# Optimization experiments

Measured on AMD Instinct MI355X. Metric: run time of the kernel, lower is better.

Reference implementation:

```python
import jax, jax.numpy as jnp
import numpy as np

N_NODES = 50000
N_EDGES = 800000
N_FEAT = 128
NHID = 64
B = 512          # num graphs
K = 30           # sort-pool k
N_CLASSES = 10


def _sage(x, src, dst, Wl, bl, Wr, n):
    # PyG SAGEConv: out = lin_l(mean_{j in N(i)} x_j) + lin_r(x_i)
    deg = jax.ops.segment_sum(jnp.ones(src.shape[0], x.dtype), dst, num_segments=n)
    agg = jax.ops.segment_sum(x[src], dst, num_segments=n)
    agg = agg / jnp.maximum(deg, 1.0)[:, None]
    return agg @ Wl + bl + x @ Wr


def _sort_pool(x, batch, num_graphs, k):
    # sort nodes within each graph descending by last feature channel, keep top-k (zero pad)
    n, f = x.shape
    order = jnp.lexsort((-x[:, -1], batch))  # primary: batch asc, secondary: last-feat desc
    xs = x[order]
    bs = batch[order]
    counts = jax.ops.segment_sum(jnp.ones(n, jnp.int32), batch, num_segments=num_graphs)
    starts = jnp.concatenate([jnp.zeros(1, jnp.int32), jnp.cumsum(counts)[:-1]])
    rank = jnp.arange(n, dtype=jnp.int32) - starts[bs]
    valid = rank < k
    gidx = jnp.where(valid, bs, num_graphs)  # out-of-bounds -> dropped by scatter
    ridx = jnp.where(valid, rank, 0)
    out = jnp.zeros((num_graphs, k, f), x.dtype).at[gidx, ridx].set(xs)
    return out  # [B, k, f]


def setup_inputs() -> dict:
    key = jax.random.key(0)
    ks = jax.random.split(key, 16)
    d = {}
    d["x"] = jax.random.normal(ks[0], (N_NODES, N_FEAT), dtype=jnp.float32)
    d["edge_index"] = jax.random.randint(ks[1], (2, N_EDGES), 0, N_NODES, dtype=jnp.int64)
    d["batch"] = jnp.sort(jax.random.randint(ks[2], (N_NODES,), 0, B, dtype=jnp.int64))

    def lin(k, fan_in, shape):
        s = 1.0 / np.sqrt(fan_in)
        return jax.random.uniform(k, shape, jnp.float32, -s, s)

    d["W1l"] = lin(ks[3], N_FEAT, (N_FEAT, NHID)); d["b1"] = lin(ks[4], N_FEAT, (NHID,))
    d["W1r"] = lin(ks[5], N_FEAT, (N_FEAT, NHID))
    d["W2l"] = lin(ks[6], NHID, (NHID, NHID)); d["b2"] = lin(ks[7], NHID, (NHID,))
    d["W2r"] = lin(ks[8], NHID, (NHID, NHID))
    d["W3l"] = lin(ks[9], NHID, (NHID, NHID)); d["b3"] = lin(ks[10], NHID, (NHID,))
    d["W3r"] = lin(ks[11], NHID, (NHID, NHID))
    d["convw"] = lin(ks[12], NHID * 5, (32, NHID, 5))  # OIH
    d["convb"] = lin(ks[13], NHID * 5, (32,))
    d["lin1w"] = lin(ks[14], 32 * 26, (32 * 26, NHID)); d["lin1b"] = lin(ks[14], 32 * 26, (NHID,))
    d["lin2w"] = lin(ks[15], NHID, (NHID, N_CLASSES)); d["lin2b"] = lin(ks[15], NHID, (N_CLASSES,))
    return d


def reference(x, edge_index, batch, W1l, b1, W1r, W2l, b2, W2r, W3l, b3, W3r,
              convw, convb, lin1w, lin1b, lin2w, lin2b):
    src, dst = edge_index[0], edge_index[1]
    h = jax.nn.relu(_sage(x, src, dst, W1l, b1, W1r, N_NODES))
    h = jax.nn.relu(_sage(h, src, dst, W2l, b2, W2r, N_NODES))
    h = jax.nn.relu(_sage(h, src, dst, W3l, b3, W3r, N_NODES))
    p = _sort_pool(h, batch, B, K)            # [B, K, NHID]
    p = jnp.transpose(p, (0, 2, 1))           # [B, NHID, K]
    c = jax.lax.conv_general_dilated(p, convw, (1,), 'VALID',
                                     dimension_numbers=('NCH', 'OIH', 'NCH'))
    c = jax.nn.relu(c + convb[None, :, None])  # [B, 32, 26]
    f = c.reshape(B, -1)
    f = jax.nn.relu(f @ lin1w + lin1b)
    logits = f @ lin2w + lin2b
    return jax.nn.log_softmax(logits, axis=-1)
```

## Files before the change

kernel.cpp:

```cpp
#include <hip/hip_runtime.h>
#include <hip/hip_bf16.h>
#include <math.h>

#define NND 50000
#define NE 800000
#define NF 128
#define NH 64
#define NB 512
#define KP 30
#define NCLS 10
#define NBKT 49
#define NTILE 196
#define NG1 782
#define NSET 208

typedef __hip_bfloat16 bf16;
typedef unsigned long long u64;
typedef unsigned short ushort_t;
typedef __attribute__((ext_vector_type(8))) short bf16x8;
typedef __attribute__((ext_vector_type(4))) float f32x4;

__device__ __forceinline__ float ldF(const void* p, size_t i, int isbf){
    return isbf ? __bfloat162float(((const bf16*)p)[i]) : ((const float*)p)[i];
}

__device__ __forceinline__ ushort_t f2bf(float v){
    unsigned u = __float_as_uint(v);
    unsigned r = u + 0x7FFFu + ((u >> 16) & 1u);
    return (ushort_t)(r >> 16);
}

__device__ __forceinline__ int floatsAreBf16(const unsigned* __restrict__ xw, int tid){
    unsigned w = xw[tid & 63];
    int ex = (int)((w >> 7) & 0xFF);
    u64 m = __ballot(ex >= 100 && ex <= 140);
    return __popcll(m) >= 32;
}
__device__ __forceinline__ int intsAreI64(const int* __restrict__ ew, int tid){
    u64 m = __ballot(ew[2*(tid & 63) + 1] == 0);
    return __popcll(m) >= 48;
}

__device__ __forceinline__ int edgeSrc(const int* ei, int e, int i64){
    return i64 ? ei[2*e] : ei[e];
}
__device__ __forceinline__ int edgeDst(const int* ei, int e, int i64){
    return i64 ? ei[2*NE + 2*e] : ei[NE + e];
}

__global__ __launch_bounds__(256) void k1_kernel(
    const unsigned* __restrict__ xw, const int* __restrict__ ei,
    const int* __restrict__ batch, int* __restrict__ starts,
    const void* W1l, const void* W1r, const void* b1,
    const void* W2l, const void* W2r, const void* b2,
    const void* W3l, const void* W3r, const void* b3,
    const void* convw, const void* convb,
    const void* l1w, const void* l1b, const void* l2w, const void* l2b,
    ushort_t* __restrict__ wB1, ushort_t* __restrict__ wB2, ushort_t* __restrict__ wB3,
    float* __restrict__ b1f, float* __restrict__ b2f, float* __restrict__ b3f,
    float* __restrict__ wT, float* __restrict__ cbf,
    float* __restrict__ l1wf, float* __restrict__ l1bf,
    float* __restrict__ l2wf, float* __restrict__ l2bf,
    int* __restrict__ bcnt, int* __restrict__ dctr,
    int* __restrict__ bbase, int* __restrict__ bcur, int* __restrict__ offs)
{
    int tid = threadIdx.x;
    if (blockIdx.x < NTILE){
        __shared__ int lh[NBKT];
        __shared__ int sc[NBKT];
        __shared__ int lastFlag;
        int i64 = intsAreI64(ei, tid);
        if (tid < NBKT) lh[tid] = 0;
        __syncthreads();
        int t0 = blockIdx.x*4096;
        #pragma unroll 4
        for (int k = 0; k < 16; ++k){
            int e = t0 + k*256 + tid;
            if (e < NE) atomicAdd(&lh[edgeDst(ei,e,i64) >> 10], 1);
        }
        __syncthreads();
        if (tid < NBKT && lh[tid]) atomicAdd(&bcnt[tid], lh[tid]);
        __syncthreads();
        if (tid == 0){
            __threadfence();
            int old = atomicAdd(dctr, 1);
            lastFlag = (old == NTILE-1) ? 1 : 0;
        }
        __syncthreads();
        if (lastFlag){
            if (tid < NBKT) sc[tid] = atomicAdd(&bcnt[tid], 0);
            __syncthreads();
            if (tid == 0){
                int acc = 0;
                for (int b = 0; b < NBKT; ++b){
                    bbase[b] = acc; bcur[b] = acc; acc += sc[b];
                }
                bbase[NBKT] = acc;
                offs[NND] = NE;
            }
        }
    } else {
        int wbf = floatsAreBf16(xw, tid);
        int i64 = intsAreI64(ei, tid);
        int i = (blockIdx.x - NTILE)*256 + tid;
        if (i < NND){
            int b  = i64 ? batch[2*i] : batch[i];
            int pb = (i == 0) ? -1 : (i64 ? batch[2*(i-1)] : batch[i-1]);
            for (int g = pb+1; g <= b; ++g) starts[g] = i;
            if (i == NND-1) for (int g = b+1; g <= NB; ++g) starts[g] = NND;
        }
        {
            int j = i & 7, lane = (i >> 3) & 63, t = (i >> 9) & 7, c = i >> 12;
            int k = c*32 + (lane >> 4)*8 + j;
            int n = t*16 + (lane & 15);
            if (i < 16384){
                float v = (n < 64) ? ldF(W1l, (size_t)k*NH + n, wbf)
                                   : ldF(W1r, (size_t)k*NH + (n-64), wbf);
                wB1[i] = f2bf(v);
            }
            if (i < 8192){
                float v2 = (n < 64) ? ldF(W2l, (size_t)k*NH + n, wbf)
                                    : ldF(W2r, (size_t)k*NH + (n-64), wbf);
                float v3 = (n < 64) ? ldF(W3l, (size_t)k*NH + n, wbf)
                                    : ldF(W3r, (size_t)k*NH + (n-64), wbf);
                wB2[i] = f2bf(v2);
                wB3[i] = f2bf(v3);
            }
        }
        if (i < 64){
            b1f[i] = ldF(b1, i, wbf);
            b2f[i] = ldF(b2, i, wbf);
            b3f[i] = ldF(b3, i, wbf);
            l1bf[i] = ldF(l1b, i, wbf);
        }
        if (i < 10240){
            int o = i / 320, rem = i - o*320, ch = rem/5, h = rem - ch*5;
            wT[ch*160 + h*32 + o] = ldF(convw, i, wbf);
        }
        if (i < 53248) l1wf[i] = ldF(l1w, i, wbf);
        if (i < 640)   l2wf[i] = ldF(l2w, i, wbf);
        if (i < 32)    cbf[i]  = ldF(convb, i, wbf);
        if (i < 10)    l2bf[i] = ldF(l2b, i, wbf);
    }
}

__global__ __launch_bounds__(256) void k2_kernel(
    const void* __restrict__ x, const int* __restrict__ ei,
    const ushort_t* __restrict__ wB1, const float* __restrict__ b1f,
    ushort_t* __restrict__ ybf, float* __restrict__ z,
    int* __restrict__ bcur, int2* __restrict__ bedges)
{
    int tid = threadIdx.x;
    if (blockIdx.x < NG1){
        constexpr int K = NF, KC = K/32, RS = K + 8;
        __shared__ ushort_t hA[64*RS];
        int isbf = floatsAreBf16((const unsigned*)x, tid);
        int base = blockIdx.x * 64;
        for (int i = tid; i < 64*K; i += 256){
            int r = i / K, c = i - r*K;
            int node = base + r;
            float v = (node < NND) ? ldF(x, (size_t)node*K + c, isbf) : 0.f;
            hA[r*RS + c] = f2bf(v);
        }
        __syncthreads();
        int lane = tid & 63, w = tid >> 6;
        int n16 = lane & 15, quad = lane >> 4;
        f32x4 acc[8];
        #pragma unroll
        for (int t = 0; t < 8; ++t) acc[t] = (f32x4){0.f,0.f,0.f,0.f};
        const bf16x8* bp = (const bf16x8*)wB1;
        #pragma unroll
        for (int c = 0; c < KC; ++c){
            bf16x8 a = *(const bf16x8*)&hA[(w*16 + n16)*RS + c*32 + quad*8];
            #pragma unroll
            for (int t = 0; t < 8; ++t){
                bf16x8 b = bp[(c*8 + t)*64 + lane];
                acc[t] = __builtin_amdgcn_mfma_f32_16x16x32_bf16(a, b, acc[t], 0, 0, 0);
            }
        }
        #pragma unroll
        for (int t = 0; t < 8; ++t){
            int f = (t & 3)*16 + n16;
            float bv = (t >= 4) ? b1f[f] : 0.f;
            #pragma unroll
            for (int r = 0; r < 4; ++r){
                int node = base + w*16 + quad*4 + r;
                if (node < NND){
                    if (t < 4) ybf[(size_t)node*NH + f] = f2bf(acc[t][r]);
                    else       z[(size_t)node*NH + f] = acc[t][r] + bv;
                }
            }
        }
    } else {
        __shared__ int lh[NBKT];
        __shared__ int lcur[NBKT];
        int i64 = intsAreI64(ei, tid);
        if (tid < NBKT) lh[tid] = 0;
        __syncthreads();
        int t0 = (blockIdx.x - NG1)*4096;
        int myd[16], mys[16];
        int cnt = 0;
        #pragma unroll 4
        for (int k = 0; k < 16; ++k){
            int e = t0 + k*256 + tid;
            if (e < NE){
                int d = edgeDst(ei,e,i64), s_ = edgeSrc(ei,e,i64);
                myd[cnt] = d; mys[cnt] = s_; ++cnt;
                atomicAdd(&lh[d >> 10], 1);
            }
        }
        __syncthreads();
        if (tid < NBKT) lcur[tid] = lh[tid] ? atomicAdd(&bcur[tid], lh[tid]) : 0;
        __syncthreads();
        for (int k = 0; k < cnt; ++k){
            int b = myd[k] >> 10;
            int p = atomicAdd(&lcur[b], 1);
            bedges[p] = make_int2(mys[k], myd[k]);
        }
    }
}

__global__ __launch_bounds__(1024) void csr_finalize(const int2* __restrict__ bedges,
                                                     const int* __restrict__ bbase,
                                                     int* __restrict__ offs,
                                                     int* __restrict__ csr){
    __shared__ int hist[1024];
    int b = blockIdx.x;
    int tid = threadIdx.x;
    int dst0 = b << 10;
    int nd = NND - dst0; if (nd > 1024) nd = 1024;
    int e0 = bbase[b], e1 = bbase[b+1];
    hist[tid] = 0;
    __syncthreads();
    for (int e = e0 + tid; e < e1; e += 1024)
        atomicAdd(&hist[bedges[e].y - dst0], 1);
    __syncthreads();
    int own = hist[tid];
    for (int st = 1; st < 1024; st <<= 1){
        int v = (tid >= st) ? hist[tid-st] : 0;
        __syncthreads();
        hist[tid] += v;
        __syncthreads();
    }
    int excl = hist[tid] - own;
    if (tid < nd) offs[dst0 + tid] = e0 + excl;
    __syncthreads();
    hist[tid] = excl;
    __syncthreads();
    for (int e = e0 + tid; e < e1; e += 1024){
        int2 ed = bedges[e];
        int p = atomicAdd(&hist[ed.y - dst0], 1);
        csr[e0 + p] = ed.x;
    }
}

__device__ __forceinline__ void addbf8(uint4 u, float* a){
    a[0] += __uint_as_float(u.x << 16);
    a[1] += __uint_as_float(u.x & 0xFFFF0000u);
    a[2] += __uint_as_float(u.y << 16);
    a[3] += __uint_as_float(u.y & 0xFFFF0000u);
    a[4] += __uint_as_float(u.z << 16);
    a[5] += __uint_as_float(u.z & 0xFFFF0000u);
    a[6] += __uint_as_float(u.w << 16);
    a[7] += __uint_as_float(u.w & 0xFFFF0000u);
}

__global__ __launch_bounds__(256) void gather_mfma(
    const ushort_t* __restrict__ yb, const int* __restrict__ offs,
    const int* __restrict__ csr, const float* __restrict__ z,
    const ushort_t* __restrict__ wB, const float* __restrict__ bfp,
    ushort_t* __restrict__ ybf_out, float* __restrict__ z_out,
    ushort_t* __restrict__ ykey_out)
{
    constexpr int K = NH;
    constexpr int KC = K/32;
    constexpr int RS = K + 8;
    __shared__ ushort_t hA[64*RS];
    int tid = threadIdx.x;
    int base = blockIdx.x * 64;

    {
        int nl = tid >> 2, q = tid & 3;
        int node = base + nl;
        float acc[16];
        #pragma unroll
        for (int i = 0; i < 16; ++i) acc[i] = 0.f;
        ushort_t row[16];
        if (node < NND){
            int o0 = offs[node], o1 = offs[node+1];
            int e = o0;
            for (; e + 3 < o1; e += 4){
                int s0 = csr[e], s1 = csr[e+1], s2 = csr[e+2], s3 = csr[e+3];
                const uint4* p0 = (const uint4*)&yb[(size_t)s0*NH + q*16];
                const uint4* p1 = (const uint4*)&yb[(size_t)s1*NH + q*16];
                const uint4* p2 = (const uint4*)&yb[(size_t)s2*NH + q*16];
                const uint4* p3 = (const uint4*)&yb[(size_t)s3*NH + q*16];
                uint4 a0 = p0[0], a1 = p0[1], b0 = p1[0], b1 = p1[1];
                uint4 c0 = p2[0], c1 = p2[1], d0 = p3[0], d1 = p3[1];
                addbf8(a0, acc); addbf8(a1, acc+8);
                addbf8(b0, acc); addbf8(b1, acc+8);
                addbf8(c0, acc); addbf8(c1, acc+8);
                addbf8(d0, acc); addbf8(d1, acc+8);
            }
            for (; e < o1; ++e){
                const uint4* p0 = (const uint4*)&yb[(size_t)csr[e]*NH + q*16];
                uint4 a0 = p0[0], a1 = p0[1];
                addbf8(a0, acc); addbf8(a1, acc+8);
            }
            float dd = (float)(o1 - o0); dd = dd > 1.f ? dd : 1.f;
            float inv = 1.f / dd;
            const float4* zp = (const float4*)&z[(size_t)node*NH + q*16];
            #pragma unroll
            for (int i4 = 0; i4 < 4; ++i4){
                float4 zz = zp[i4];
                float v0 = acc[i4*4+0]*inv + zz.x;
                float v1 = acc[i4*4+1]*inv + zz.y;
                float v2 = acc[i4*4+2]*inv + zz.z;
                float v3 = acc[i4*4+3]*inv + zz.w;
                row[i4*4+0] = f2bf(v0 > 0.f ? v0 : 0.f);
                row[i4*4+1] = f2bf(v1 > 0.f ? v1 : 0.f);
                row[i4*4+2] = f2bf(v2 > 0.f ? v2 : 0.f);
                row[i4*4+3] = f2bf(v3 > 0.f ? v3 : 0.f);
            }
        } else {
            #pragma unroll
            for (int i = 0; i < 16; ++i) row[i] = 0;
        }
        unsigned pk[8];
        #pragma unroll
        for (int i = 0; i < 8; ++i)
            pk[i] = (unsigned)row[2*i] | ((unsigned)row[2*i+1] << 16);
        *(uint4*)&hA[nl*RS + q*16]     = make_uint4(pk[0],pk[1],pk[2],pk[3]);
        *(uint4*)&hA[nl*RS + q*16 + 8] = make_uint4(pk[4],pk[5],pk[6],pk[7]);
    }
    __syncthreads();

    int lane = tid & 63, w = tid >> 6;
    int n16 = lane & 15, quad = lane >> 4;
    f32x4 acc[8];
    #pragma unroll
    for (int t = 0; t < 8; ++t) acc[t] = (f32x4){0.f,0.f,0.f,0.f};
    const bf16x8* bp = (const bf16x8*)wB;
    #pragma unroll
    for (int c = 0; c < KC; ++c){
        bf16x8 a = *(const bf16x8*)&hA[(w*16 + n16)*RS + c*32 + quad*8];
        #pragma unroll
        for (int t = 0; t < 8; ++t){
            bf16x8 b = bp[(c*8 + t)*64 + lane];
            acc[t] = __builtin_amdgcn_mfma_f32_16x16x32_bf16(a, b, acc[t], 0, 0, 0);
        }
    }
    #pragma unroll
    for (int t = 0; t < 8; ++t){
        int f = (t & 3)*16 + n16;
        float bv = (t >= 4) ? bfp[f] : 0.f;
        #pragma unroll
        for (int r = 0; r < 4; ++r){
            int node = base + w*16 + quad*4 + r;
            if (node < NND){
                if (t < 4){
                    ushort_t yv = f2bf(acc[t][r]);
                    ybf_out[(size_t)node*NH + f] = yv;
                    if (ykey_out != nullptr && t == 3 && n16 == 15)
                        ykey_out[node] = yv;
                } else {
                    z_out[(size_t)node*NH + f] = acc[t][r] + bv;
                }
            }
        }
    }
}

__device__ __forceinline__ void acc4(uint2 u, float& a0, float& a1, float& a2, float& a3){
    a0 += __uint_as_float(u.x << 16);
    a1 += __uint_as_float(u.x & 0xFFFF0000u);
    a2 += __uint_as_float(u.y << 16);
    a3 += __uint_as_float(u.y & 0xFFFF0000u);
}

__global__ __launch_bounds__(256) void head4_kernel(
    const ushort_t* __restrict__ yb, const ushort_t* __restrict__ ykey,
    const int* __restrict__ offs, const int* __restrict__ csr,
    const float* __restrict__ z, const int* __restrict__ starts,
    const float* __restrict__ wT, const float* __restrict__ cbf,
    const float* __restrict__ l1wf, const float* __restrict__ l1bf,
    const float* __restrict__ l2wf, const float* __restrict__ l2bf,
    float* __restrict__ outp)
{
    __shared__ u64  keys[256];
    __shared__ int  sel[KP];
    __shared__ float pT[64*32];
    __shared__ float part[8*832];
    __shared__ float cbuf[832];
    __shared__ float fbuf[NH];
    __shared__ float logitsS[NCLS];
    int g = blockIdx.x, tid = threadIdx.x;
    int s = starts[g], e = starts[g+1];
    int cnt = e - s; if (cnt > 256) cnt = 256; if (cnt < 0) cnt = 0;

    u64 key = 0xFFFFFFFFFFFFFFFFull;
    if (tid < cnt){
        int node = s + tid;
        int o0 = offs[node], o1 = offs[node+1];
        float a = 0.f;
        int ee = o0;
        for (; ee + 3 < o1; ee += 4){
            float v0 = __uint_as_float((unsigned)ykey[csr[ee+0]] << 16);
            float v1 = __uint_as_float((unsigned)ykey[csr[ee+1]] << 16);
            float v2 = __uint_as_float((unsigned)ykey[csr[ee+2]] << 16);
            float v3 = __uint_as_float((unsigned)ykey[csr[ee+3]] << 16);
            a += v0; a += v1; a += v2; a += v3;
        }
        for (; ee < o1; ++ee)
            a += __uint_as_float((unsigned)ykey[csr[ee]] << 16);
        float dd = (float)(o1 - o0); dd = dd > 1.f ? dd : 1.f;
        float inv = 1.f / dd;
        float v = a*inv + z[(size_t)node*NH + 63];
        v = v > 0.f ? v : 0.f;
        unsigned u = __float_as_uint(v);
        unsigned m = (u & 0x80000000u) ? ~u : (u | 0x80000000u);
        unsigned d = ~m;
        key = ((u64)d << 32) | (unsigned)tid;
    }
    keys[tid] = key;
    __syncthreads();
    for (int k = 2; k <= 256; k <<= 1){
        for (int j = k >> 1; j > 0; j >>= 1){
            int partner = tid ^ j;
            u64 a = keys[tid], b = keys[partner];
            bool up = ((tid & k) == 0);
            bool amin = a < b;
            u64 keep;
            if (partner > tid) keep = (up == amin) ? a : b;
            else               keep = (up == amin) ? b : a;
            __syncthreads();
            keys[tid] = keep;
            __syncthreads();
        }
    }
    if (tid < KP){
        u64 kk = keys[tid];
        sel[tid] = ((unsigned)(kk >> 32) == 0xFFFFFFFFu) ? -1 : (int)(kk & 0xFFFFFFFFu);
    }
    if (tid < 64){ pT[tid*32 + 30] = 0.f; pT[tid*32 + 31] = 0.f; }
    __syncthreads();

    #pragma unroll
    for (int r0 = 0; r0 < 32; r0 += 16){
        int r = r0 + (tid >> 4);
        int q = tid & 15;
        if (r < KP){
            float4 v = make_float4(0.f,0.f,0.f,0.f);
            int li = sel[r];
            if (li >= 0){
                int node = s + li;
                int o0 = offs[node], o1 = offs[node+1];
                float a0=0.f, a1=0.f, a2=0.f, a3=0.f;
                int ee = o0;
                for (; ee + 3 < o1; ee += 4){
                    int s0 = csr[ee], s1 = csr[ee+1], s2 = csr[ee+2], s3 = csr[ee+3];
                    uint2 u0 = *(const uint2*)&yb[(size_t)s0*NH + q*4];
                    uint2 u1 = *(const uint2*)&yb[(size_t)s1*NH + q*4];
                    uint2 u2 = *(const uint2*)&yb[(size_t)s2*NH + q*4];
                    uint2 u3 = *(const uint2*)&yb[(size_t)s3*NH + q*4];
                    acc4(u0, a0,a1,a2,a3); acc4(u1, a0,a1,a2,a3);
                    acc4(u2, a0,a1,a2,a3); acc4(u3, a0,a1,a2,a3);
                }
                for (; ee < o1; ++ee){
                    uint2 u = *(const uint2*)&yb[(size_t)csr[ee]*NH + q*4];
                    acc4(u, a0,a1,a2,a3);
                }
                float dd = (float)(o1 - o0); dd = dd > 1.f ? dd : 1.f;
                float inv = 1.f / dd;
                float4 zz = *(const float4*)&z[(size_t)node*NH + q*4];
                v.x = a0*inv + zz.x; v.y = a1*inv + zz.y;
                v.z = a2*inv + zz.z; v.w = a3*inv + zz.w;
                v.x = v.x > 0.f ? v.x : 0.f;  v.y = v.y > 0.f ? v.y : 0.f;
                v.z = v.z > 0.f ? v.z : 0.f;  v.w = v.w > 0.f ? v.w : 0.f;
            }
            pT[(q*4+0)*32 + r] = v.x;
            pT[(q*4+1)*32 + r] = v.y;
            pT[(q*4+2)*32 + r] = v.z;
            pT[(q*4+3)*32 + r] = v.w;
        }
    }
    __syncthreads();

    int o = tid & 31, chg = tid >> 5;
    float acc[26];
    #pragma unroll
    for (int t = 0; t < 26; ++t) acc[t] = 0.f;
    for (int c8 = 0; c8 < 8; ++c8){
        int ch = chg*8 + c8;
        const float4* prow = (const float4*)&pT[ch*32];
        float p[32];
        #pragma unroll
        for (int q = 0; q < 8; ++q){
            float4 v = prow[q];
            p[4*q]=v.x; p[4*q+1]=v.y; p[4*q+2]=v.z; p[4*q+3]=v.w;
        }
        const float* wrow = &wT[ch*160 + o];
        #pragma unroll
        for (int h = 0; h < 5; ++h){
            float wv = wrow[h*32];
            #pragma unroll
            for (int t = 0; t < 26; ++t) acc[t] += p[t+h]*wv;
        }
    }
    #pragma unroll
    for (int t = 0; t < 26; ++t) part[chg*832 + o*26 + t] = acc[t];
    __syncthreads();

    for (int i = tid; i < 832; i += 256){
        int oo = i / 26;
        float a = cbf[oo];
        #pragma unroll
        for (int cg = 0; cg < 8; ++cg) a += part[cg*832 + i];
        cbuf[i] = a > 0.f ? a : 0.f;
    }
    __syncthreads();

    {
        int p = tid >> 6, j = tid & 63;
        float a = 0.f;
        int m0 = p*208;
        #pragma unroll 4
        for (int m = m0; m < m0 + 208; ++m)
            a += cbuf[m] * l1wf[(size_t)m*NH + j];
        part[p*NH + j] = a;
    }
    __syncthreads();
    if (tid < NH){
        float v = part[tid] + part[NH+tid] + part[2*NH+tid] + part[3*NH+tid] + l1bf[tid];
        fbuf[tid] = v > 0.f ? v : 0.f;
    }
    __syncthreads();
    if (tid < NCLS){
        float a = l2bf[tid];
        #pragma unroll
        for (int j = 0; j < NH; ++j) a += fbuf[j] * l2wf[j*NCLS + tid];
        logitsS[tid] = a;
    }
    __syncthreads();
    if (tid == 0){
        float m = logitsS[0];
        for (int c = 1; c < NCLS; ++c) m = fmaxf(m, logitsS[c]);
        float ssum = 0.f;
        for (int c = 0; c < NCLS; ++c) ssum += expf(logitsS[c]-m);
        float lse = m + logf(ssum);
        for (int c = 0; c < NCLS; ++c)
            outp[(size_t)g*NCLS + c] = logitsS[c] - lse;
    }
}

extern "C" void kernel_launch(void* const* d_in, const int* in_sizes, int n_in,
                              void* d_out, int out_size, void* d_ws, size_t ws_size,
                              hipStream_t stream) {
    const void* x    = d_in[0];
    const int*  ei   = (const int*)d_in[1];
    const int*  batch= (const int*)d_in[2];
    const void *W1l=d_in[3], *b1=d_in[4],  *W1r=d_in[5];
    const void *W2l=d_in[6], *b2=d_in[7],  *W2r=d_in[8];
    const void *W3l=d_in[9], *b3=d_in[10], *W3r=d_in[11];
    const void *convw=d_in[12], *convb=d_in[13];
    const void *l1w=d_in[14], *l1b=d_in[15];
    const void *l2w=d_in[16], *l2b=d_in[17];
    float* out = (float*)d_out;

    float* wsf = (float*)d_ws;
    ushort_t* yA = (ushort_t*)wsf;
    float* zA  = wsf + (size_t)NND*NH/2;
    ushort_t* yB = (ushort_t*)(zA + (size_t)NND*NH);
    float* zB  = (float*)(yB + (size_t)NND*NH);
    int2* bedges = (int2*)(zB + (size_t)NND*NH);
    ushort_t* wB1 = (ushort_t*)(bedges + NE);
    ushort_t* wB2 = wB1 + 16384;
    ushort_t* wB3 = wB2 + 8192;
    ushort_t* ykey = wB3 + 8192;
    float* b1f  = (float*)(ykey + NND + 8);
    float* b2f  = b1f + 64;
    float* b3f  = b2f + 64;
    float* wT   = b3f + 64;
    float* cbf  = wT + 10240;
    float* l1wf = cbf + 32;
    float* l1bf = l1wf + 53248;
    float* l2wf = l1bf + 64;
    float* l2bf = l2wf + 640;
    int* starts = (int*)(l2bf + 16);
    int* bcnt   = starts + 520;
    int* dctr   = bcnt + NBKT;
    int* bbase  = bcnt + 64;
    int* bcur   = bbase + 64;
    int* offs   = bcur + 64;
    int* csr    = offs + NND + 3;

    (void)hipMemsetAsync(bcnt, 0, 50*sizeof(int), stream);

    k1_kernel<<<NTILE + NSET, 256, 0, stream>>>(
        (const unsigned*)x, ei, batch, starts,
        W1l, W1r, b1, W2l, W2r, b2, W3l, W3r, b3,
        convw, convb, l1w, l1b, l2w, l2b,
        wB1, wB2, wB3, b1f, b2f, b3f,
        wT, cbf, l1wf, l1bf, l2wf, l2bf,
        bcnt, dctr, bbase, bcur, offs);

    k2_kernel<<<NG1 + NTILE, 256, 0, stream>>>(
        x, ei, wB1, b1f, yA, zA, bcur, bedges);

    csr_finalize<<<NBKT, 1024, 0, stream>>>(bedges, bbase, offs, csr);

    gather_mfma<<<NG1, 256, 0, stream>>>(yA, offs, csr, zA, wB2, b2f, yB, zB, nullptr);
    gather_mfma<<<NG1, 256, 0, stream>>>(yB, offs, csr, zB, wB3, b3f, yA, zA, ykey);

    head4_kernel<<<NB, 256, 0, stream>>>(yA, ykey, offs, csr, zA, starts,
                                         wT, cbf, l1wf, l1bf, l2wf, l2bf, out);
}
```

Measured before the change: 260.8 us.

## Store self-term z buffers in bf16 and restructure head conv partials

The per-node self-term z (x@Wr + b) is now written and read as bf16 instead of fp32 in all layers and the head, halving its memory traffic. Separately, the head kernel's conv stage is reorganized: each thread computes 13 output positions over 16 channels instead of 26 over 8, so partial sums need 4 slices rather than 8. That partial buffer now shares shared memory with the sort keys, cutting LDS use and allowing more blocks per CU. The trade-off is extra rounding error in z, which could shift the top-k sort order near ties.

```diff
diff --git a/kernel.cpp b/kernel.cpp
--- a/kernel.cpp
+++ b/kernel.cpp
@@ -29,6 +29,8 @@
     unsigned r = u + 0x7FFFu + ((u >> 16) & 1u);
     return (ushort_t)(r >> 16);
 }
+__device__ __forceinline__ float bfLo(unsigned w){ return __uint_as_float(w << 16); }
+__device__ __forceinline__ float bfHi(unsigned w){ return __uint_as_float(w & 0xFFFF0000u); }
 
 __device__ __forceinline__ int floatsAreBf16(const unsigned* __restrict__ xw, int tid){
     unsigned w = xw[tid & 63];
@@ -147,7 +149,7 @@
 __global__ __launch_bounds__(256) void k2_kernel(
     const void* __restrict__ x, const int* __restrict__ ei,
     const ushort_t* __restrict__ wB1, const float* __restrict__ b1f,
-    ushort_t* __restrict__ ybf, float* __restrict__ z,
+    ushort_t* __restrict__ ybf, ushort_t* __restrict__ zb,
     int* __restrict__ bcur, int2* __restrict__ bedges)
 {
     int tid = threadIdx.x;
@@ -187,7 +189,7 @@
                 int node = base + w*16 + quad*4 + r;
                 if (node < NND){
                     if (t < 4) ybf[(size_t)node*NH + f] = f2bf(acc[t][r]);
-                    else       z[(size_t)node*NH + f] = acc[t][r] + bv;
+                    else       zb[(size_t)node*NH + f] = f2bf(acc[t][r] + bv);
                 }
             }
         }
@@ -255,21 +257,23 @@
 }
 
 __device__ __forceinline__ void addbf8(uint4 u, float* a){
-    a[0] += __uint_as_float(u.x << 16);
-    a[1] += __uint_as_float(u.x & 0xFFFF0000u);
-    a[2] += __uint_as_float(u.y << 16);
-    a[3] += __uint_as_float(u.y & 0xFFFF0000u);
-    a[4] += __uint_as_float(u.z << 16);
-    a[5] += __uint_as_float(u.z & 0xFFFF0000u);
-    a[6] += __uint_as_float(u.w << 16);
-    a[7] += __uint_as_float(u.w & 0xFFFF0000u);
+    a[0] += bfLo(u.x); a[1] += bfHi(u.x);
+    a[2] += bfLo(u.y); a[3] += bfHi(u.y);
+    a[4] += bfLo(u.z); a[5] += bfHi(u.z);
+    a[6] += bfLo(u.w); a[7] += bfHi(u.w);
+}
+__device__ __forceinline__ void decbf8(uint4 u, float* o){
+    o[0] = bfLo(u.x); o[1] = bfHi(u.x);
+    o[2] = bfLo(u.y); o[3] = bfHi(u.y);
+    o[4] = bfLo(u.z); o[5] = bfHi(u.z);
+    o[6] = bfLo(u.w); o[7] = bfHi(u.w);
 }
 
 __global__ __launch_bounds__(256) void gather_mfma(
     const ushort_t* __restrict__ yb, const int* __restrict__ offs,
-    const int* __restrict__ csr, const float* __restrict__ z,
+    const int* __restrict__ csr, const ushort_t* __restrict__ zb,
     const ushort_t* __restrict__ wB, const float* __restrict__ bfp,
-    ushort_t* __restrict__ ybf_out, float* __restrict__ z_out,
+    ushort_t* __restrict__ ybf_out, ushort_t* __restrict__ zb_out,
     ushort_t* __restrict__ ykey_out)
 {
     constexpr int K = NH;
@@ -309,18 +313,14 @@
             }
             float dd = (float)(o1 - o0); dd = dd > 1.f ? dd : 1.f;
             float inv = 1.f / dd;
-            const float4* zp = (const float4*)&z[(size_t)node*NH + q*16];
+            const uint4* zp = (const uint4*)&zb[(size_t)node*NH + q*16];
+            uint4 zu0 = zp[0], zu1 = zp[1];
+            float zf[16];
+            decbf8(zu0, zf); decbf8(zu1, zf+8);
             #pragma unroll
-            for (int i4 = 0; i4 < 4; ++i4){
-                float4 zz = zp[i4];
-                float v0 = acc[i4*4+0]*inv + zz.x;
-                float v1 = acc[i4*4+1]*inv + zz.y;
-                float v2 = acc[i4*4+2]*inv + zz.z;
-                float v3 = acc[i4*4+3]*inv + zz.w;
-                row[i4*4+0] = f2bf(v0 > 0.f ? v0 : 0.f);
-                row[i4*4+1] = f2bf(v1 > 0.f ? v1 : 0.f);
-                row[i4*4+2] = f2bf(v2 > 0.f ? v2 : 0.f);
-                row[i4*4+3] = f2bf(v3 > 0.f ? v3 : 0.f);
+            for (int i = 0; i < 16; ++i){
+                float v = acc[i]*inv + zf[i];
+                row[i] = f2bf(v > 0.f ? v : 0.f);
             }
         } else {
             #pragma unroll
@@ -364,7 +364,7 @@
                     if (ykey_out != nullptr && t == 3 && n16 == 15)
                         ykey_out[node] = yv;
                 } else {
-                    z_out[(size_t)node*NH + f] = acc[t][r] + bv;
+                    zb_out[(size_t)node*NH + f] = f2bf(acc[t][r] + bv);
                 }
             }
         }
@@ -372,25 +372,24 @@
 }
 
 __device__ __forceinline__ void acc4(uint2 u, float& a0, float& a1, float& a2, float& a3){
-    a0 += __uint_as_float(u.x << 16);
-    a1 += __uint_as_float(u.x & 0xFFFF0000u);
-    a2 += __uint_as_float(u.y << 16);
-    a3 += __uint_as_float(u.y & 0xFFFF0000u);
-}
-
-__global__ __launch_bounds__(256) void head4_kernel(
+    a0 += bfLo(u.x); a1 += bfHi(u.x);
+    a2 += bfLo(u.y); a3 += bfHi(u.y);
+}
+
+__global__ __launch_bounds__(256) void head5_kernel(
     const ushort_t* __restrict__ yb, const ushort_t* __restrict__ ykey,
     const int* __restrict__ offs, const int* __restrict__ csr,
-    const float* __restrict__ z, const int* __restrict__ starts,
+    const ushort_t* __restrict__ zb, const int* __restrict__ starts,
     const float* __restrict__ wT, const float* __restrict__ cbf,
     const float* __restrict__ l1wf, const float* __restrict__ l1bf,
     const float* __restrict__ l2wf, const float* __restrict__ l2bf,
     float* __restrict__ outp)
 {
-    __shared__ u64  keys[256];
-    __shared__ int  sel[KP];
+    __shared__ double scratch8[1664];
+    u64*   keys  = (u64*)scratch8;
+    float* part4 = (float*)scratch8;
+    __shared__ int  sel[32];
     __shared__ float pT[64*32];
-    __shared__ float part[8*832];
     __shared__ float cbuf[832];
     __shared__ float fbuf[NH];
     __shared__ float logitsS[NCLS];
@@ -405,17 +404,17 @@
         float a = 0.f;
         int ee = o0;
         for (; ee + 3 < o1; ee += 4){
-            float v0 = __uint_as_float((unsigned)ykey[csr[ee+0]] << 16);
-            float v1 = __uint_as_float((unsigned)ykey[csr[ee+1]] << 16);
-            float v2 = __uint_as_float((unsigned)ykey[csr[ee+2]] << 16);
-            float v3 = __uint_as_float((unsigned)ykey[csr[ee+3]] << 16);
+            float v0 = bfLo((unsigned)ykey[csr[ee+0]]);
+            float v1 = bfLo((unsigned)ykey[csr[ee+1]]);
+            float v2 = bfLo((unsigned)ykey[csr[ee+2]]);
+            float v3 = bfLo((unsigned)ykey[csr[ee+3]]);
             a += v0; a += v1; a += v2; a += v3;
         }
         for (; ee < o1; ++ee)
-            a += __uint_as_float((unsigned)ykey[csr[ee]] << 16);
+            a += bfLo((unsigned)ykey[csr[ee]]);
         float dd = (float)(o1 - o0); dd = dd > 1.f ? dd : 1.f;
         float inv = 1.f / dd;
-        float v = a*inv + z[(size_t)node*NH + 63];
+        float v = a*inv + bfLo((unsigned)zb[(size_t)node*NH + 63]);
         v = v > 0.f ? v : 0.f;
         unsigned u = __float_as_uint(v);
         unsigned m = (u & 0x80000000u) ? ~u : (u | 0x80000000u);
@@ -472,9 +471,9 @@
                 }
                 float dd = (float)(o1 - o0); dd = dd > 1.f ? dd : 1.f;
                 float inv = 1.f / dd;
-                float4 zz = *(const float4*)&z[(size_t)node*NH + q*4];
-                v.x = a0*inv + zz.x; v.y = a1*inv + zz.y;
-                v.z = a2*inv + zz.z; v.w = a3*inv + zz.w;
+                uint2 zu = *(const uint2*)&zb[(size_t)node*NH + q*4];
+                v.x = a0*inv + bfLo(zu.x); v.y = a1*inv + bfHi(zu.x);
+                v.z = a2*inv + bfLo(zu.y); v.w = a3*inv + bfHi(zu.y);
                 v.x = v.x > 0.f ? v.x : 0.f;  v.y = v.y > 0.f ? v.y : 0.f;
                 v.z = v.z > 0.f ? v.z : 0.f;  v.w = v.w > 0.f ? v.w : 0.f;
             }
@@ -486,36 +485,41 @@
     }
     __syncthreads();
 
-    int o = tid & 31, chg = tid >> 5;
-    float acc[26];
-    #pragma unroll
-    for (int t = 0; t < 26; ++t) acc[t] = 0.f;
-    for (int c8 = 0; c8 < 8; ++c8){
-        int ch = chg*8 + c8;
-        const float4* prow = (const float4*)&pT[ch*32];
-        float p[32];
-        #pragma unroll
-        for (int q = 0; q < 8; ++q){
-            float4 v = prow[q];
-            p[4*q]=v.x; p[4*q+1]=v.y; p[4*q+2]=v.z; p[4*q+3]=v.w;
-        }
-        const float* wrow = &wT[ch*160 + o];
-        #pragma unroll
-        for (int h = 0; h < 5; ++h){
-            float wv = wrow[h*32];
+    {
+        int lane = tid & 63, chg4 = tid >> 6;
+        int o = lane & 31, th = lane >> 5;
+        int t0 = th ? 13 : 0;
+        int f4s = th ? 3 : 0;
+        int poff = th ? 1 : 0;
+        float acc[13];
+        #pragma unroll
+        for (int t = 0; t < 13; ++t) acc[t] = 0.f;
+        for (int c16 = 0; c16 < 16; ++c16){
+            int ch = chg4*16 + c16;
+            const float4* prow = (const float4*)&pT[ch*32];
+            float p[20];
             #pragma unroll
-            for (int t = 0; t < 26; ++t) acc[t] += p[t+h]*wv;
-        }
-    }
-    #pragma unroll
-    for (int t = 0; t < 26; ++t) part[chg*832 + o*26 + t] = acc[t];
+            for (int j = 0; j < 5; ++j){
+                float4 v = prow[f4s + j];
+                p[4*j]=v.x; p[4*j+1]=v.y; p[4*j+2]=v.z; p[4*j+3]=v.w;
+            }
+            const float* wrow = &wT[ch*160 + o];
+            #pragma unroll
+            for (int h = 0; h < 5; ++h){
+                float wv = wrow[h*32];
+                #pragma unroll
+                for (int t = 0; t < 13; ++t) acc[t] += p[t+h+poff]*wv;
+            }
+        }
+        #pragma unroll
+        for (int t = 0; t < 13; ++t)
+            part4[chg4*832 + o*26 + t0 + t] = acc[t];
+    }
     __syncthreads();
 
     for (int i = tid; i < 832; i += 256){
         int oo = i / 26;
-        float a = cbf[oo];
-        #pragma unroll
-        for (int cg = 0; cg < 8; ++cg) a += part[cg*832 + i];
+        float a = cbf[oo] + part4[i] + part4[832+i] + part4[2*832+i] + part4[3*832+i];
         cbuf[i] = a > 0.f ? a : 0.f;
     }
     __syncthreads();
@@ -527,11 +531,11 @@
         #pragma unroll 4
         for (int m = m0; m < m0 + 208; ++m)
             a += cbuf[m] * l1wf[(size_t)m*NH + j];
-        part[p*NH + j] = a;
+        part4[p*NH + j] = a;
     }
     __syncthreads();
     if (tid < NH){
-        float v = part[tid] + part[NH+tid] + part[2*NH+tid] + part[3*NH+tid] + l1bf[tid];
+        float v = part4[tid] + part4[NH+tid] + part4[2*NH+tid] + part4[3*NH+tid] + l1bf[tid];
         fbuf[tid] = v > 0.f ? v : 0.f;
     }
     __syncthreads();
@@ -569,9 +573,9 @@
 
     float* wsf = (float*)d_ws;
     ushort_t* yA = (ushort_t*)wsf;
-    float* zA  = wsf + (size_t)NND*NH/2;
-    ushort_t* yB = (ushort_t*)(zA + (size_t)NND*NH);
-    float* zB  = (float*)(yB + (size_t)NND*NH);
+    ushort_t* zA = yA + (size_t)NND*NH;
+    ushort_t* yB = zA + (size_t)NND*NH;
+    ushort_t* zB = yB + (size_t)NND*NH;
     int2* bedges = (int2*)(zB + (size_t)NND*NH);
     ushort_t* wB1 = (ushort_t*)(bedges + NE);
     ushort_t* wB2 = wB1 + 16384;
@@ -612,6 +616,6 @@
     gather_mfma<<<NG1, 256, 0, stream>>>(yA, offs, csr, zA, wB2, b2f, yB, zB, nullptr);
     gather_mfma<<<NG1, 256, 0, stream>>>(yB, offs, csr, zB, wB3, b3f, yA, zA, ykey);
 
-    head4_kernel<<<NB, 256, 0, stream>>>(yA, ykey, offs, csr, zA, starts,
+    head5_kernel<<<NB, 256, 0, stream>>>(yA, ykey, offs, csr, zA, starts,
                                          wT, cbf, l1wf, l1bf, l2wf, l2bf, out);
 }
```

Measured after the change: 380.2 us. 1.46x slower.
